# Optimization experiments

Hardware: AMD Instinct MI355X
Metric: run time of the kernel (lower is better)

The kernel has to match this reference:

```python
import jax, jax.numpy as jnp
import numpy as np

WIDTH = 256
FREQS = 10
INPUT_WIDTH = 3 + 3 * 2 * FREQS  # 63


def embed_point(point, freqs):
    # point: [N, 3] -> [N, 3*(1+2*freqs)]
    linear = point[..., None]                                  # [N, 3, 1]
    scales = jnp.exp2(jnp.arange(freqs, dtype=point.dtype))    # [freqs]
    angles = linear * scales                                   # [N, 3, freqs]
    emb = jnp.concatenate((linear, jnp.sin(angles), jnp.cos(angles)), axis=-1)
    return emb.reshape(*point.shape[:-1], 3 * (1 + 2 * freqs))


def _xavier(key, fan_in, fan_out):
    limit = jnp.sqrt(6.0 / (fan_in + fan_out)).astype(jnp.float32)
    return jax.random.uniform(key, (fan_in, fan_out), jnp.float32, -limit, limit)


def setup_inputs() -> dict:
    key = jax.random.key(0)
    keys = jax.random.split(key, 20)
    N = 524288
    point = jax.random.normal(keys[0], (N, 3), dtype=jnp.float32)
    dims = [
        (INPUT_WIDTH, WIDTH), (WIDTH, WIDTH), (WIDTH, WIDTH), (WIDTH, WIDTH),
        (WIDTH, WIDTH), (WIDTH + INPUT_WIDTH, WIDTH), (WIDTH, WIDTH),
        (WIDTH, WIDTH), (WIDTH, 4),
    ]
    inp = {"point": point}
    for i, (fi, fo) in enumerate(dims):
        inp[f"w{i}"] = _xavier(keys[1 + i], fi, fo)
        inp[f"b{i}"] = jnp.zeros((fo,), dtype=jnp.float32)
    return inp


def reference(point, w0, b0, w1, b1, w2, b2, w3, b3, w4, b4,
              w5, b5, w6, b6, w7, b7, w8, b8):
    inp = embed_point(point, FREQS)                 # [N, 63]
    x = jax.nn.relu(inp @ w0 + b0)
    x = jax.nn.relu(x @ w1 + b1)
    x = jax.nn.relu(x @ w2 + b2)
    x = jax.nn.relu(x @ w3 + b3)
    x = jax.nn.relu(x @ w4 + b4)
    x = jax.nn.relu(jnp.concatenate((x, inp), -1) @ w5 + b5)  # skip concat
    x = jax.nn.relu(x @ w6 + b6)
    x = jax.nn.relu(x @ w7 + b7)
    return x @ w8 + b8                              # [N, 4]
```

## Files before the change

kernel.cpp:

```cpp
#include <hip/hip_runtime.h>
#include <math.h>


typedef __attribute__((ext_vector_type(8))) short short8;
typedef __attribute__((ext_vector_type(4))) float f32x4;
typedef __attribute__((ext_vector_type(16))) float f32x16;

struct WPtrs { const float* w[8]; };
struct BPtrs { const float* b[8]; };

#define INV2PI 0.15915494309189533577f

#define PK_L0 0
#define PK_L1 16384
#define PK_L2 81920
#define PK_L3 147456
#define PK_L4 212992
#define PK_L5 278528
#define PK_L6 360448
#define PK_L7 425984
#define PK_W8 491520
#define PK_TOTAL 495616

__device__ __forceinline__ unsigned short f2bf(float v) {
  unsigned u = __float_as_uint(v);
  u = u + 0x7fffu + ((u >> 16) & 1u);
  return (unsigned short)(u >> 16);
}
__device__ __forceinline__ float bf_lo(unsigned u) { return __uint_as_float(u << 16); }
__device__ __forceinline__ float bf_hi(unsigned u) { return __uint_as_float(u & 0xffff0000u); }

__device__ __forceinline__ unsigned cvtpk(float a, float b) {
#if __has_builtin(__builtin_amdgcn_cvt_pk_bf16_f32)
  typedef __attribute__((ext_vector_type(2))) __bf16 bf16x2_t;
  bf16x2_t r = __builtin_amdgcn_cvt_pk_bf16_f32(a, b);
  return __builtin_bit_cast(unsigned, r);
#else
  unsigned ua = __float_as_uint(a);
  ua += 0x7fffu + ((ua >> 16) & 1u);
  unsigned ub = __float_as_uint(b);
  ub += 0x7fffu + ((ub >> 16) & 1u);
#if __has_builtin(__builtin_amdgcn_perm)
  return __builtin_amdgcn_perm(ub, ua, 0x07060302u);
#else
  return (ua >> 16) | (ub & 0xffff0000u);
#endif
#endif
}

__device__ __forceinline__ float fractf_(float x) {
#if __has_builtin(__builtin_amdgcn_fract_f32)
  return __builtin_amdgcn_fract_f32(x);
#else
  return x - floorf(x);
#endif
}
__device__ __forceinline__ float sin_rev(float rev) {
#if __has_builtin(__builtin_amdgcn_sinf)
  return __builtin_amdgcn_sinf(rev);
#else
  return __sinf(rev * 6.283185307179586f);
#endif
}

__device__ __forceinline__ float embval(int f, float c0, float c1, float c2,
                                        float x0, float x1, float x2) {
  if (f >= 63) return 0.0f;
  int d = (f >= 21 ? 1 : 0) + (f >= 42 ? 1 : 0);
  int r = f - d * 21;
  float c = (d == 0) ? c0 : (d == 1 ? c1 : c2);
  float x = (d == 0) ? x0 : (d == 1 ? x1 : x2);
  bool isc = r > 10;
  int e = isc ? (r - 11) : (r - 1);
  float rev = fractf_(ldexpf(x, e) + (isc ? 0.25f : 0.0f));
  float s = sin_rev(rev);
  return (r == 0) ? c : s;
}

__device__ __forceinline__ f32x16 mfma32(short8 a, short8 b, f32x16 c) {
  return __builtin_amdgcn_mfma_f32_32x32x16_bf16(a, b, c, 0, 0, 0);
}
__device__ __forceinline__ f32x4 mfma16(short8 a, short8 b, f32x4 c) {
  return __builtin_amdgcn_mfma_f32_16x16x32_bf16(a, b, c, 0, 0, 0);
}

__global__ void pack_weights(WPtrs W, const float* __restrict__ w8,
                             unsigned short* __restrict__ out) {
  int idx = blockIdx.x * 256 + threadIdx.x;
  if (idx >= PK_TOTAL) return;
  float v;
  if (idx >= PK_W8) {
    int t = idx - PK_W8;
    int j = t >> 8, k = t & 255;
    v = (j < 4) ? w8[k * 4 + j] : 0.0f;
  } else {
    int e = idx & 15;
    int blk = idx >> 4;
    int ch = blk & 255;
    int kkg = blk >> 8;
    int l, kk0;
    if      (kkg < 4)   { l = 0; kk0 = 0;   }
    else if (kkg < 20)  { l = 1; kk0 = 4;   }
    else if (kkg < 36)  { l = 2; kk0 = 20;  }
    else if (kkg < 52)  { l = 3; kk0 = 36;  }
    else if (kkg < 68)  { l = 4; kk0 = 52;  }
    else if (kkg < 88)  { l = 5; kk0 = 68;  }
    else if (kkg < 104) { l = 6; kk0 = 88;  }
    else                { l = 7; kk0 = 104; }
    int k = (kkg - kk0) * 16 + e;
    const int realK[8] = {63, 256, 256, 256, 256, 319, 256, 256};
    v = (k < realK[l]) ? W.w[l][k * 256 + ch] : 0.0f;
  }
  out[idx] = f2bf(v);
}

template <int KKA, int PAB, int KKB, bool RB>
__device__ __forceinline__ void do_layer32(
    const unsigned short* srcA, const unsigned short* srcB,
    const unsigned short* __restrict__ wblk,
    const float* __restrict__ bias,
    unsigned short* dst, int w, int n, int h, unsigned swz) {
  f32x16 acc[2][4];
#pragma unroll
  for (int mt = 0; mt < 2; ++mt)
#pragma unroll
    for (int q = 0; q < 4; ++q) {
      f32x4 bq = *reinterpret_cast<const f32x4*>(bias + w * 64 + mt * 32 + q * 8 + h * 4);
#pragma unroll
      for (int nt = 0; nt < 4; ++nt)
#pragma unroll
        for (int r = 0; r < 4; ++r)
          acc[mt][nt][q * 4 + r] = bq[r];
    }

  const char* wb = (const char*)wblk;
  const unsigned aoff = (unsigned)(((w * 64 + n) * 16 + h * 8) * 2);
  const char* rA = (const char*)srcA + (unsigned)(n * PAB);

#pragma unroll 4
  for (int kk = 0; kk < KKA; ++kk) {
    short8 a0 = *reinterpret_cast<const short8*>(wb + (aoff + (unsigned)(kk * 8192)));
    short8 a1 = *reinterpret_cast<const short8*>(wb + (aoff + (unsigned)(kk * 8192 + 1024)));
    unsigned off = ((unsigned)(kk * 32 + h * 16)) ^ swz;
    const char* p = rA + off;
    short8 b0 = *reinterpret_cast<const short8*>(p);
    short8 b1 = *reinterpret_cast<const short8*>(p + 32 * PAB);
    short8 b2 = *reinterpret_cast<const short8*>(p + 64 * PAB);
    short8 b3 = *reinterpret_cast<const short8*>(p + 96 * PAB);
    acc[0][0] = mfma32(a0, b0, acc[0][0]);
    acc[0][1] = mfma32(a0, b1, acc[0][1]);
    acc[0][2] = mfma32(a0, b2, acc[0][2]);
    acc[0][3] = mfma32(a0, b3, acc[0][3]);
    acc[1][0] = mfma32(a1, b0, acc[1][0]);
    acc[1][1] = mfma32(a1, b1, acc[1][1]);
    acc[1][2] = mfma32(a1, b2, acc[1][2]);
    acc[1][3] = mfma32(a1, b3, acc[1][3]);
  }
  if (KKB > 0) {
    const char* rB = (const char*)srcB + (unsigned)(n * 128);
#pragma unroll
    for (int kl = 0; kl < KKB; ++kl) {
      const char* ab2 = wb + (aoff + (unsigned)((KKA + kl) * 8192));
      short8 a0 = *reinterpret_cast<const short8*>(ab2);
      short8 a1 = *reinterpret_cast<const short8*>(ab2 + 1024);
      unsigned off = ((unsigned)(kl * 32 + h * 16)) ^ swz;
      const char* p = rB + off;
      short8 b0 = *reinterpret_cast<const short8*>(p);
      short8 b1 = *reinterpret_cast<const short8*>(p + 32 * 128);
      short8 b2 = *reinterpret_cast<const short8*>(p + 64 * 128);
      short8 b3 = *reinterpret_cast<const short8*>(p + 96 * 128);
      acc[0][0] = mfma32(a0, b0, acc[0][0]);
      acc[0][1] = mfma32(a0, b1, acc[0][1]);
      acc[0][2] = mfma32(a0, b2, acc[0][2]);
      acc[0][3] = mfma32(a0, b3, acc[0][3]);
      acc[1][0] = mfma32(a1, b0, acc[1][0]);
      acc[1][1] = mfma32(a1, b1, acc[1][1]);
      acc[1][2] = mfma32(a1, b2, acc[1][2]);
      acc[1][3] = mfma32(a1, b3, acc[1][3]);
    }
  }

  if (RB) __syncthreads();
  char* d0 = (char*)dst + (unsigned)(n * 512);
#pragma unroll
  for (int mt = 0; mt < 2; ++mt)
#pragma unroll
    for (int q = 0; q < 4; ++q) {
      unsigned soff = ((unsigned)(w * 128 + mt * 64 + q * 16 + h * 8)) ^ swz;
      char* sp = d0 + soff;
#pragma unroll
      for (int nt = 0; nt < 4; ++nt) {
        float x0 = fmaxf(acc[mt][nt][q * 4 + 0], 0.0f);
        float x1 = fmaxf(acc[mt][nt][q * 4 + 1], 0.0f);
        float x2 = fmaxf(acc[mt][nt][q * 4 + 2], 0.0f);
        float x3 = fmaxf(acc[mt][nt][q * 4 + 3], 0.0f);
        uint2 pr;
        pr.x = cvtpk(x0, x1);
        pr.y = cvtpk(x2, x3);
        *reinterpret_cast<uint2*>(sp + nt * 16384) = pr;
      }
    }
  __syncthreads();
}

__launch_bounds__(256, 2)
__global__ void mlp_mfma(const float* __restrict__ pts, long N,
                         BPtrs B, const float* __restrict__ b8,
                         const unsigned short* __restrict__ wpk,
                         float* __restrict__ out) {
  extern __shared__ unsigned short smem[];
  unsigned short* act = smem;
  unsigned short* emb = smem + 32768;
  const int tid = threadIdx.x;
  const int w = tid >> 6, lane = tid & 63;
  const int n = lane & 31, h = lane >> 5;
  const unsigned swz = (unsigned)((n & 7) << 4);
  const long pbase = (long)blockIdx.x * 128;

  {
    const int pt = tid >> 1, fg = tid & 1;
    const long pg = pbase + pt;
    float c0 = 0.f, c1 = 0.f, c2 = 0.f;
    if (pg < N) {
      const float* pp = pts + pg * 3;
      c0 = __builtin_nontemporal_load(pp);
      c1 = __builtin_nontemporal_load(pp + 1);
      c2 = __builtin_nontemporal_load(pp + 2);
    }
    float x0 = c0 * INV2PI, x1 = c1 * INV2PI, x2 = c2 * INV2PI;
    const unsigned sw = (unsigned)((pt & 7) << 4);
    char* rowp = (char*)emb + (unsigned)(pt * 128);
#pragma unroll
    for (int jb = 0; jb < 2; ++jb) {
      unsigned pk[8];
#pragma unroll
      for (int i = 0; i < 16; i += 2) {
        int f0 = fg * 32 + jb * 16 + i;
        float v0 = embval(f0,     c0, c1, c2, x0, x1, x2);
        float v1 = embval(f0 + 1, c0, c1, c2, x0, x1, x2);
        pk[i >> 1] = cvtpk(v0, v1);
      }
      unsigned base = (unsigned)(fg * 64 + jb * 32);
      *reinterpret_cast<uint4*>(rowp + (base ^ sw)) =
          uint4{pk[0], pk[1], pk[2], pk[3]};
      *reinterpret_cast<uint4*>(rowp + ((base + 16) ^ sw)) =
          uint4{pk[4], pk[5], pk[6], pk[7]};
    }
  }
  __syncthreads();

  do_layer32<4,  128, 0, false>(emb, nullptr, wpk + PK_L0, B.b[0], act, w, n, h, swz);
  do_layer32<16, 512, 0, true >(act, nullptr, wpk + PK_L1, B.b[1], act, w, n, h, swz);
  do_layer32<16, 512, 0, true >(act, nullptr, wpk + PK_L2, B.b[2], act, w, n, h, swz);
  do_layer32<16, 512, 0, true >(act, nullptr, wpk + PK_L3, B.b[3], act, w, n, h, swz);
  do_layer32<16, 512, 0, true >(act, nullptr, wpk + PK_L4, B.b[4], act, w, n, h, swz);
  do_layer32<16, 512, 4, true >(act, emb,     wpk + PK_L5, B.b[5], act, w, n, h, swz);
  do_layer32<16, 512, 0, true >(act, nullptr, wpk + PK_L6, B.b[6], act, w, n, h, swz);
  do_layer32<16, 512, 0, true >(act, nullptr, wpk + PK_L7, B.b[7], act, w, n, h, swz);

  {
    const int l16 = lane & 15, quad = lane >> 4;
    const unsigned short* w8b = wpk + PK_W8 + (unsigned)(l16 * 256 + quad * 8);
    short8 wf[8];
#pragma unroll
    for (int kk = 0; kk < 8; ++kk)
      wf[kk] = *reinterpret_cast<const short8*>(w8b + kk * 32);
    f32x4 bb = *reinterpret_cast<const f32x4*>(b8);
#pragma unroll
    for (int it = 0; it < 2; ++it) {
      const int pt = w * 32 + it * 16 + l16;
      const char* ba = (const char*)act + (unsigned)(pt * 512);
      f32x4 a4 = {0.f, 0.f, 0.f, 0.f};
#pragma unroll
      for (int kk = 0; kk < 8; ++kk) {
        unsigned off = ((unsigned)(kk * 64 + quad * 16)) ^ swz;
        short8 b = *reinterpret_cast<const short8*>(ba + off);
        a4 = mfma16(wf[kk], b, a4);
      }
      if (quad == 0) {
        long pg = pbase + pt;
        f32x4 v = a4 + bb;
        if (pg < N)
          __builtin_nontemporal_store(v, reinterpret_cast<f32x4*>(out + pg * 4));
      }
    }
  }
}

__device__ __forceinline__ unsigned pk2s(float a, float b) {
  return (unsigned)f2bf(a) | ((unsigned)f2bf(b) << 16);
}
__device__ __forceinline__ void fb_seg(const unsigned short* src, int kRows,
                                       const float* __restrict__ wr,
                                       int lane, int ps, float acc[4][16]) {
#pragma unroll 4
  for (int k = 0; k < kRows; ++k) {
    const float* p = wr + k * 256 + lane;
    float w0 = p[0], w1 = p[64], w2 = p[128], w3 = p[192];
    const uint4* xr = reinterpret_cast<const uint4*>(src + ((k << 6) + ps));
    uint4 q0 = xr[0], q1 = xr[1];
    float x[16];
    x[0] = bf_lo(q0.x);  x[1] = bf_hi(q0.x);  x[2] = bf_lo(q0.y);  x[3] = bf_hi(q0.y);
    x[4] = bf_lo(q0.z);  x[5] = bf_hi(q0.z);  x[6] = bf_lo(q0.w);  x[7] = bf_hi(q0.w);
    x[8] = bf_lo(q1.x);  x[9] = bf_hi(q1.x);  x[10] = bf_lo(q1.y); x[11] = bf_hi(q1.y);
    x[12] = bf_lo(q1.z); x[13] = bf_hi(q1.z); x[14] = bf_lo(q1.w); x[15] = bf_hi(q1.w);
#pragma unroll
    for (int pp = 0; pp < 16; ++pp) {
      acc[0][pp] = fmaf(w0, x[pp], acc[0][pp]);
      acc[1][pp] = fmaf(w1, x[pp], acc[1][pp]);
      acc[2][pp] = fmaf(w2, x[pp], acc[2][pp]);
      acc[3][pp] = fmaf(w3, x[pp], acc[3][pp]);
    }
  }
}
__device__ __forceinline__ void fb_layer(const unsigned short* srcA, int kA,
                                         const unsigned short* srcB, int kB,
                                         const float* wrA, const float* wrB,
                                         const float* bias,
                                         unsigned short* dst, int lane, int ps) {
  float acc[4][16];
#pragma unroll
  for (int jt = 0; jt < 4; ++jt) {
    float bb = bias[lane + (jt << 6)];
#pragma unroll
    for (int pp = 0; pp < 16; ++pp) acc[jt][pp] = bb;
  }
  fb_seg(srcA, kA, wrA, lane, ps, acc);
  if (srcB) fb_seg(srcB, kB, wrB, lane, ps, acc);
#pragma unroll
  for (int jt = 0; jt < 4; ++jt) {
    unsigned short* dr = dst + (((lane + (jt << 6)) << 6) + ps);
    float r[16];
#pragma unroll
    for (int pp = 0; pp < 16; ++pp) r[pp] = fmaxf(acc[jt][pp], 0.0f);
    uint4 a, b;
    a.x = pk2s(r[0], r[1]);   a.y = pk2s(r[2], r[3]);
    a.z = pk2s(r[4], r[5]);   a.w = pk2s(r[6], r[7]);
    b.x = pk2s(r[8], r[9]);   b.y = pk2s(r[10], r[11]);
    b.z = pk2s(r[12], r[13]); b.w = pk2s(r[14], r[15]);
    reinterpret_cast<uint4*>(dr)[0] = a;
    reinterpret_cast<uint4*>(dr)[1] = b;
  }
}
__launch_bounds__(256, 2)
__global__ void mlp_fallback(const float* __restrict__ pts, int N,
                             WPtrs W, BPtrs B,
                             const float* __restrict__ w8,
                             const float* __restrict__ b8,
                             float* __restrict__ out) {
  __shared__ unsigned short act[256 * 64];
  __shared__ unsigned short emb[64 * 64];
  const int lane = threadIdx.x & 63;
  const int ps = (threadIdx.x >> 6) << 4;
  const long pbase = (long)blockIdx.x * 64 + ps;
#pragma unroll
  for (int i = 0; i < 16; ++i) {
    int idx = (i << 6) + lane;
    int f = idx >> 4, pp = idx & 15;
    float v = 0.0f;
    if (f < 63) {
      float c = (pbase + pp < N) ? pts[(pbase + pp) * 3 + (f / 21)] : 0.0f;
      float x = c * INV2PI;
      v = embval(f, c, c, c, x, x, x);
    }
    emb[(f << 6) + ps + pp] = f2bf(v);
  }
  fb_layer(emb, 63, nullptr, 0, W.w[0], nullptr, B.b[0], act, lane, ps);
#pragma unroll 1
  for (int l = 1; l <= 4; ++l)
    fb_layer(act, 256, nullptr, 0, W.w[l], nullptr, B.b[l], act, lane, ps);
  fb_layer(act, 256, emb, 63, W.w[5], W.w[5] + 256 * 256, B.b[5], act, lane, ps);
#pragma unroll 1
  for (int l = 6; l <= 7; ++l)
    fb_layer(act, 256, nullptr, 0, W.w[l], nullptr, B.b[l], act, lane, ps);
  {
    const int pp = lane & 15, cc = lane >> 4;
    float a = b8[cc];
#pragma unroll 4
    for (int k = 0; k < 256; ++k)
      a = fmaf(bf_lo((unsigned)act[(k << 6) + ps + pp]), w8[(k << 2) + cc], a);
    if (pbase + pp < N) out[(pbase + pp) * 4 + cc] = a;
  }
}

extern "C" void kernel_launch(void* const* d_in, const int* in_sizes, int n_in,
                              void* d_out, int out_size, void* d_ws, size_t ws_size,
                              hipStream_t stream) {
  const float* pts = (const float*)d_in[0];
  WPtrs W; BPtrs B;
  for (int i = 0; i < 8; ++i) {
    W.w[i] = (const float*)d_in[1 + 2 * i];
    B.b[i] = (const float*)d_in[2 + 2 * i];
  }
  const float* w8 = (const float*)d_in[17];
  const float* b8 = (const float*)d_in[18];
  float* out = (float*)d_out;
  const long N = in_sizes[0] / 3;

  const size_t need = (size_t)PK_TOTAL * sizeof(unsigned short);
  if (ws_size >= need) {
    static hipError_t attr_err = hipFuncSetAttribute(
        reinterpret_cast<const void*>(mlp_mfma),
        hipFuncAttributeMaxDynamicSharedMemorySize, 81920);
    if (attr_err == hipSuccess) {
      unsigned short* wpk = (unsigned short*)d_ws;
      pack_weights<<<1936, 256, 0, stream>>>(W, w8, wpk);
      mlp_mfma<<<(int)((N + 127) / 128), 256, 81920, stream>>>(pts, N, B, b8, wpk, out);
      return;
    }
  }
  mlp_fallback<<<(int)((N + 63) / 64), 256, 0, stream>>>(pts, (int)N, W, B, w8, b8, out);
}
```

Measured before the change: 551.9 us.

## Split MLP tile across eight waves and ping-pong activation buffers

Doubles the block to 512 threads and splits each layer's output tile over a 4x2 wave grid, so each wave holds half as many accumulators. Activations now alternate between two LDS buffers, which drops the pre-writeback barrier in each layer. The embedding stage is also redistributed over four threads per point. In exchange, LDS per block grows to 144KB, which likely allows only one block per CU, and each weight fragment fetched from global memory feeds half as many MFMAs.

New measurement: 698.8 us. 26.6% more time.

```diff
diff --git a/kernel.cpp b/kernel.cpp
--- a/kernel.cpp
+++ b/kernel.cpp
@@ -114,28 +114,28 @@
   out[idx] = f2bf(v);
 }
 
-template <int KKA, int PAB, int KKB, bool RB>
+template <int KKA, int PAB, int KKB>
 __device__ __forceinline__ void do_layer32(
     const unsigned short* srcA, const unsigned short* srcB,
     const unsigned short* __restrict__ wblk,
     const float* __restrict__ bias,
-    unsigned short* dst, int w, int n, int h, unsigned swz) {
-  f32x16 acc[2][4];
+    unsigned short* dst, int wr, int wc, int n, int h, unsigned swz) {
+  f32x16 acc[2][2];
 #pragma unroll
   for (int mt = 0; mt < 2; ++mt)
 #pragma unroll
     for (int q = 0; q < 4; ++q) {
-      f32x4 bq = *reinterpret_cast<const f32x4*>(bias + w * 64 + mt * 32 + q * 8 + h * 4);
-#pragma unroll
-      for (int nt = 0; nt < 4; ++nt)
+      f32x4 bq = *reinterpret_cast<const f32x4*>(bias + wr * 64 + mt * 32 + q * 8 + h * 4);
+#pragma unroll
+      for (int nt = 0; nt < 2; ++nt)
 #pragma unroll
         for (int r = 0; r < 4; ++r)
           acc[mt][nt][q * 4 + r] = bq[r];
     }
 
   const char* wb = (const char*)wblk;
-  const unsigned aoff = (unsigned)(((w * 64 + n) * 16 + h * 8) * 2);
-  const char* rA = (const char*)srcA + (unsigned)(n * PAB);
+  const unsigned aoff = (unsigned)((wr * 64 + n) * 32 + h * 16);
+  const char* rA = (const char*)srcA + (unsigned)((wc * 64 + n) * PAB);
 
 #pragma unroll 4
   for (int kk = 0; kk < KKA; ++kk) {
@@ -145,19 +145,13 @@
     const char* p = rA + off;
     short8 b0 = *reinterpret_cast<const short8*>(p);
     short8 b1 = *reinterpret_cast<const short8*>(p + 32 * PAB);
-    short8 b2 = *reinterpret_cast<const short8*>(p + 64 * PAB);
-    short8 b3 = *reinterpret_cast<const short8*>(p + 96 * PAB);
     acc[0][0] = mfma32(a0, b0, acc[0][0]);
     acc[0][1] = mfma32(a0, b1, acc[0][1]);
-    acc[0][2] = mfma32(a0, b2, acc[0][2]);
-    acc[0][3] = mfma32(a0, b3, acc[0][3]);
     acc[1][0] = mfma32(a1, b0, acc[1][0]);
     acc[1][1] = mfma32(a1, b1, acc[1][1]);
-    acc[1][2] = mfma32(a1, b2, acc[1][2]);
-    acc[1][3] = mfma32(a1, b3, acc[1][3]);
   }
   if (KKB > 0) {
-    const char* rB = (const char*)srcB + (unsigned)(n * 128);
+    const char* rB = (const char*)srcB + (unsigned)((wc * 64 + n) * 128);
 #pragma unroll
     for (int kl = 0; kl < KKB; ++kl) {
       const char* ab2 = wb + (aoff + (unsigned)((KKA + kl) * 8192));
@@ -167,29 +161,22 @@
       const char* p = rB + off;
       short8 b0 = *reinterpret_cast<const short8*>(p);
       short8 b1 = *reinterpret_cast<const short8*>(p + 32 * 128);
-      short8 b2 = *reinterpret_cast<const short8*>(p + 64 * 128);
-      short8 b3 = *reinterpret_cast<const short8*>(p + 96 * 128);
       acc[0][0] = mfma32(a0, b0, acc[0][0]);
       acc[0][1] = mfma32(a0, b1, acc[0][1]);
-      acc[0][2] = mfma32(a0, b2, acc[0][2]);
-      acc[0][3] = mfma32(a0, b3, acc[0][3]);
       acc[1][0] = mfma32(a1, b0, acc[1][0]);
       acc[1][1] = mfma32(a1, b1, acc[1][1]);
-      acc[1][2] = mfma32(a1, b2, acc[1][2]);
-      acc[1][3] = mfma32(a1, b3, acc[1][3]);
-    }
-  }
-
-  if (RB) __syncthreads();
-  char* d0 = (char*)dst + (unsigned)(n * 512);
+    }
+  }
+
+  char* d0 = (char*)dst + (unsigned)((wc * 64 + n) * 512);
 #pragma unroll
   for (int mt = 0; mt < 2; ++mt)
 #pragma unroll
     for (int q = 0; q < 4; ++q) {
-      unsigned soff = ((unsigned)(w * 128 + mt * 64 + q * 16 + h * 8)) ^ swz;
+      unsigned soff = ((unsigned)(wr * 128 + mt * 64 + q * 16 + h * 8)) ^ swz;
       char* sp = d0 + soff;
 #pragma unroll
-      for (int nt = 0; nt < 4; ++nt) {
+      for (int nt = 0; nt < 2; ++nt) {
         float x0 = fmaxf(acc[mt][nt][q * 4 + 0], 0.0f);
         float x1 = fmaxf(acc[mt][nt][q * 4 + 1], 0.0f);
         float x2 = fmaxf(acc[mt][nt][q * 4 + 2], 0.0f);
@@ -203,22 +190,24 @@
   __syncthreads();
 }
 
-__launch_bounds__(256, 2)
+__launch_bounds__(512, 2)
 __global__ void mlp_mfma(const float* __restrict__ pts, long N,
                          BPtrs B, const float* __restrict__ b8,
                          const unsigned short* __restrict__ wpk,
                          float* __restrict__ out) {
   extern __shared__ unsigned short smem[];
-  unsigned short* act = smem;
-  unsigned short* emb = smem + 32768;
+  unsigned short* act0 = smem;
+  unsigned short* act1 = smem + 32768;
+  unsigned short* emb  = smem + 65536;
   const int tid = threadIdx.x;
   const int w = tid >> 6, lane = tid & 63;
   const int n = lane & 31, h = lane >> 5;
+  const int wr = w >> 1, wc = w & 1;
   const unsigned swz = (unsigned)((n & 7) << 4);
   const long pbase = (long)blockIdx.x * 128;
 
   {
-    const int pt = tid >> 1, fg = tid & 1;
+    const int pt = tid >> 2, fg = tid & 3;
     const long pg = pbase + pt;
     float c0 = 0.f, c1 = 0.f, c2 = 0.f;
     if (pg < N) {
@@ -228,35 +217,31 @@
       c2 = __builtin_nontemporal_load(pp + 2);
     }
     float x0 = c0 * INV2PI, x1 = c1 * INV2PI, x2 = c2 * INV2PI;
+    unsigned pk[8];
+#pragma unroll
+    for (int i = 0; i < 16; i += 2) {
+      int f0 = fg * 16 + i;
+      float v0 = embval(f0,     c0, c1, c2, x0, x1, x2);
+      float v1 = embval(f0 + 1, c0, c1, c2, x0, x1, x2);
+      pk[i >> 1] = cvtpk(v0, v1);
+    }
     const unsigned sw = (unsigned)((pt & 7) << 4);
     char* rowp = (char*)emb + (unsigned)(pt * 128);
-#pragma unroll
-    for (int jb = 0; jb < 2; ++jb) {
-      unsigned pk[8];
-#pragma unroll
-      for (int i = 0; i < 16; i += 2) {
-        int f0 = fg * 32 + jb * 16 + i;
-        float v0 = embval(f0,     c0, c1, c2, x0, x1, x2);
-        float v1 = embval(f0 + 1, c0, c1, c2, x0, x1, x2);
-        pk[i >> 1] = cvtpk(v0, v1);
-      }
-      unsigned base = (unsigned)(fg * 64 + jb * 32);
-      *reinterpret_cast<uint4*>(rowp + (base ^ sw)) =
-          uint4{pk[0], pk[1], pk[2], pk[3]};
-      *reinterpret_cast<uint4*>(rowp + ((base + 16) ^ sw)) =
-          uint4{pk[4], pk[5], pk[6], pk[7]};
-    }
+    *reinterpret_cast<uint4*>(rowp + (((unsigned)(fg * 32)) ^ sw)) =
+        uint4{pk[0], pk[1], pk[2], pk[3]};
+    *reinterpret_cast<uint4*>(rowp + (((unsigned)(fg * 32 + 16)) ^ sw)) =
+        uint4{pk[4], pk[5], pk[6], pk[7]};
   }
   __syncthreads();
 
-  do_layer32<4,  128, 0, false>(emb, nullptr, wpk + PK_L0, B.b[0], act, w, n, h, swz);
-  do_layer32<16, 512, 0, true >(act, nullptr, wpk + PK_L1, B.b[1], act, w, n, h, swz);
-  do_layer32<16, 512, 0, true >(act, nullptr, wpk + PK_L2, B.b[2], act, w, n, h, swz);
-  do_layer32<16, 512, 0, true >(act, nullptr, wpk + PK_L3, B.b[3], act, w, n, h, swz);
-  do_layer32<16, 512, 0, true >(act, nullptr, wpk + PK_L4, B.b[4], act, w, n, h, swz);
-  do_layer32<16, 512, 4, true >(act, emb,     wpk + PK_L5, B.b[5], act, w, n, h, swz);
-  do_layer32<16, 512, 0, true >(act, nullptr, wpk + PK_L6, B.b[6], act, w, n, h, swz);
-  do_layer32<16, 512, 0, true >(act, nullptr, wpk + PK_L7, B.b[7], act, w, n, h, swz);
+  do_layer32<4,  128, 0>(emb,  nullptr, wpk + PK_L0, B.b[0], act0, wr, wc, n, h, swz);
+  do_layer32<16, 512, 0>(act0, nullptr, wpk + PK_L1, B.b[1], act1, wr, wc, n, h, swz);
+  do_layer32<16, 512, 0>(act1, nullptr, wpk + PK_L2, B.b[2], act0, wr, wc, n, h, swz);
+  do_layer32<16, 512, 0>(act0, nullptr, wpk + PK_L3, B.b[3], act1, wr, wc, n, h, swz);
+  do_layer32<16, 512, 0>(act1, nullptr, wpk + PK_L4, B.b[4], act0, wr, wc, n, h, swz);
+  do_layer32<16, 512, 4>(act0, emb,     wpk + PK_L5, B.b[5], act1, wr, wc, n, h, swz);
+  do_layer32<16, 512, 0>(act1, nullptr, wpk + PK_L6, B.b[6], act0, wr, wc, n, h, swz);
+  do_layer32<16, 512, 0>(act0, nullptr, wpk + PK_L7, B.b[7], act1, wr, wc, n, h, swz);
 
   {
     const int l16 = lane & 15, quad = lane >> 4;
@@ -266,23 +251,20 @@
     for (int kk = 0; kk < 8; ++kk)
       wf[kk] = *reinterpret_cast<const short8*>(w8b + kk * 32);
     f32x4 bb = *reinterpret_cast<const f32x4*>(b8);
-#pragma unroll
-    for (int it = 0; it < 2; ++it) {
-      const int pt = w * 32 + it * 16 + l16;
-      const char* ba = (const char*)act + (unsigned)(pt * 512);
-      f32x4 a4 = {0.f, 0.f, 0.f, 0.f};
-#pragma unroll
-      for (int kk = 0; kk < 8; ++kk) {
-        unsigned off = ((unsigned)(kk * 64 + quad * 16)) ^ swz;
-        short8 b = *reinterpret_cast<const short8*>(ba + off);
-        a4 = mfma16(wf[kk], b, a4);
-      }
-      if (quad == 0) {
-        long pg = pbase + pt;
-        f32x4 v = a4 + bb;
-        if (pg < N)
-          __builtin_nontemporal_store(v, reinterpret_cast<f32x4*>(out + pg * 4));
-      }
+    const int pt = w * 16 + l16;
+    const char* ba = (const char*)act1 + (unsigned)(pt * 512);
+    f32x4 a4 = {0.f, 0.f, 0.f, 0.f};
+#pragma unroll
+    for (int kk = 0; kk < 8; ++kk) {
+      unsigned off = ((unsigned)(kk * 64 + quad * 16)) ^ swz;
+      short8 b = *reinterpret_cast<const short8*>(ba + off);
+      a4 = mfma16(wf[kk], b, a4);
+    }
+    if (quad == 0) {
+      long pg = pbase + pt;
+      f32x4 v = a4 + bb;
+      if (pg < N)
+        __builtin_nontemporal_store(v, reinterpret_cast<f32x4*>(out + pg * 4));
     }
   }
 }
@@ -401,11 +383,11 @@
   if (ws_size >= need) {
     static hipError_t attr_err = hipFuncSetAttribute(
         reinterpret_cast<const void*>(mlp_mfma),
-        hipFuncAttributeMaxDynamicSharedMemorySize, 81920);
+        hipFuncAttributeMaxDynamicSharedMemorySize, 147456);
     if (attr_err == hipSuccess) {
       unsigned short* wpk = (unsigned short*)d_ws;
       pack_weights<<<1936, 256, 0, stream>>>(W, w8, wpk);
-      mlp_mfma<<<(int)((N + 127) / 128), 256, 81920, stream>>>(pts, N, B, b8, wpk, out);
+      mlp_mfma<<<(int)((N + 127) / 128), 512, 147456, stream>>>(pts, N, B, b8, wpk, out);
       return;
     }
   }
```

## Split warps into 2x2 grid over output channels and points in MLP layers

Applied to the files above, without the earlier changes.

Changes the per-wave tile in each layer from 64 channels x 128 points to 128 channels x 64 points, arranging the four waves as a 2x2 grid. Each k-step now loads four weight fragments from global/L2 and two activation fragments from LDS instead of two and four. That halves LDS activation reads per MFMA but doubles per-wave weight fragment loads from global memory, which may add latency and cache pressure.

After: 635.7 us. 15.2% more time.

```diff
diff --git a/kernel.cpp b/kernel.cpp
--- a/kernel.cpp
+++ b/kernel.cpp
@@ -119,77 +119,78 @@
     const unsigned short* srcA, const unsigned short* srcB,
     const unsigned short* __restrict__ wblk,
     const float* __restrict__ bias,
-    unsigned short* dst, int w, int n, int h, unsigned swz) {
-  f32x16 acc[2][4];
-#pragma unroll
-  for (int mt = 0; mt < 2; ++mt)
+    unsigned short* dst, int wr, int wc, int n, int h, unsigned swz) {
+  f32x16 acc[4][2];
+#pragma unroll
+  for (int mt = 0; mt < 4; ++mt)
 #pragma unroll
     for (int q = 0; q < 4; ++q) {
-      f32x4 bq = *reinterpret_cast<const f32x4*>(bias + w * 64 + mt * 32 + q * 8 + h * 4);
-#pragma unroll
-      for (int nt = 0; nt < 4; ++nt)
+      f32x4 bq = *reinterpret_cast<const f32x4*>(bias + wr * 128 + mt * 32 + q * 8 + h * 4);
+#pragma unroll
+      for (int nt = 0; nt < 2; ++nt)
 #pragma unroll
         for (int r = 0; r < 4; ++r)
           acc[mt][nt][q * 4 + r] = bq[r];
     }
 
   const char* wb = (const char*)wblk;
-  const unsigned aoff = (unsigned)(((w * 64 + n) * 16 + h * 8) * 2);
-  const char* rA = (const char*)srcA + (unsigned)(n * PAB);
-
-#pragma unroll 4
+  const unsigned aoff = (unsigned)((wr * 128 + n) * 32 + h * 16);
+  const char* rA = (const char*)srcA + (unsigned)((wc * 64 + n) * PAB);
+
+#pragma unroll 2
   for (int kk = 0; kk < KKA; ++kk) {
-    short8 a0 = *reinterpret_cast<const short8*>(wb + (aoff + (unsigned)(kk * 8192)));
-    short8 a1 = *reinterpret_cast<const short8*>(wb + (aoff + (unsigned)(kk * 8192 + 1024)));
+    const char* ap = wb + (aoff + (unsigned)(kk * 8192));
+    short8 a0 = *reinterpret_cast<const short8*>(ap);
+    short8 a1 = *reinterpret_cast<const short8*>(ap + 1024);
+    short8 a2 = *reinterpret_cast<const short8*>(ap + 2048);
+    short8 a3 = *reinterpret_cast<const short8*>(ap + 3072);
     unsigned off = ((unsigned)(kk * 32 + h * 16)) ^ swz;
     const char* p = rA + off;
     short8 b0 = *reinterpret_cast<const short8*>(p);
     short8 b1 = *reinterpret_cast<const short8*>(p + 32 * PAB);
-    short8 b2 = *reinterpret_cast<const short8*>(p + 64 * PAB);
-    short8 b3 = *reinterpret_cast<const short8*>(p + 96 * PAB);
     acc[0][0] = mfma32(a0, b0, acc[0][0]);
     acc[0][1] = mfma32(a0, b1, acc[0][1]);
-    acc[0][2] = mfma32(a0, b2, acc[0][2]);
-    acc[0][3] = mfma32(a0, b3, acc[0][3]);
     acc[1][0] = mfma32(a1, b0, acc[1][0]);
     acc[1][1] = mfma32(a1, b1, acc[1][1]);
-    acc[1][2] = mfma32(a1, b2, acc[1][2]);
-    acc[1][3] = mfma32(a1, b3, acc[1][3]);
+    acc[2][0] = mfma32(a2, b0, acc[2][0]);
+    acc[2][1] = mfma32(a2, b1, acc[2][1]);
+    acc[3][0] = mfma32(a3, b0, acc[3][0]);
+    acc[3][1] = mfma32(a3, b1, acc[3][1]);
   }
   if (KKB > 0) {
-    const char* rB = (const char*)srcB + (unsigned)(n * 128);
+    const char* rB = (const char*)srcB + (unsigned)((wc * 64 + n) * 128);
 #pragma unroll
     for (int kl = 0; kl < KKB; ++kl) {
-      const char* ab2 = wb + (aoff + (unsigned)((KKA + kl) * 8192));
-      short8 a0 = *reinterpret_cast<const short8*>(ab2);
-      short8 a1 = *reinterpret_cast<const short8*>(ab2 + 1024);
+      const char* ap = wb + (aoff + (unsigned)((KKA + kl) * 8192));
+      short8 a0 = *reinterpret_cast<const short8*>(ap);
+      short8 a1 = *reinterpret_cast<const short8*>(ap + 1024);
+      short8 a2 = *reinterpret_cast<const short8*>(ap + 2048);
+      short8 a3 = *reinterpret_cast<const short8*>(ap + 3072);
       unsigned off = ((unsigned)(kl * 32 + h * 16)) ^ swz;
       const char* p = rB + off;
       short8 b0 = *reinterpret_cast<const short8*>(p);
       short8 b1 = *reinterpret_cast<const short8*>(p + 32 * 128);
-      short8 b2 = *reinterpret_cast<const short8*>(p + 64 * 128);
-      short8 b3 = *reinterpret_cast<const short8*>(p + 96 * 128);
       acc[0][0] = mfma32(a0, b0, acc[0][0]);
       acc[0][1] = mfma32(a0, b1, acc[0][1]);
-      acc[0][2] = mfma32(a0, b2, acc[0][2]);
-      acc[0][3] = mfma32(a0, b3, acc[0][3]);
       acc[1][0] = mfma32(a1, b0, acc[1][0]);
       acc[1][1] = mfma32(a1, b1, acc[1][1]);
-      acc[1][2] = mfma32(a1, b2, acc[1][2]);
-      acc[1][3] = mfma32(a1, b3, acc[1][3]);
+      acc[2][0] = mfma32(a2, b0, acc[2][0]);
+      acc[2][1] = mfma32(a2, b1, acc[2][1]);
+      acc[3][0] = mfma32(a3, b0, acc[3][0]);
+      acc[3][1] = mfma32(a3, b1, acc[3][1]);
     }
   }
 
   if (RB) __syncthreads();
-  char* d0 = (char*)dst + (unsigned)(n * 512);
-#pragma unroll
-  for (int mt = 0; mt < 2; ++mt)
+  char* d0 = (char*)dst + (unsigned)((wc * 64 + n) * 512);
+#pragma unroll
+  for (int mt = 0; mt < 4; ++mt)
 #pragma unroll
     for (int q = 0; q < 4; ++q) {
-      unsigned soff = ((unsigned)(w * 128 + mt * 64 + q * 16 + h * 8)) ^ swz;
+      unsigned soff = ((unsigned)(wr * 256 + mt * 64 + q * 16 + h * 8)) ^ swz;
       char* sp = d0 + soff;
 #pragma unroll
-      for (int nt = 0; nt < 4; ++nt) {
+      for (int nt = 0; nt < 2; ++nt) {
         float x0 = fmaxf(acc[mt][nt][q * 4 + 0], 0.0f);
         float x1 = fmaxf(acc[mt][nt][q * 4 + 1], 0.0f);
         float x2 = fmaxf(acc[mt][nt][q * 4 + 2], 0.0f);
@@ -214,6 +215,7 @@
   const int tid = threadIdx.x;
   const int w = tid >> 6, lane = tid & 63;
   const int n = lane & 31, h = lane >> 5;
+  const int wr = w >> 1, wc = w & 1;
   const unsigned swz = (unsigned)((n & 7) << 4);
   const long pbase = (long)blockIdx.x * 128;
 
@@ -249,14 +251,14 @@
   }
   __syncthreads();
 
-  do_layer32<4,  128, 0, false>(emb, nullptr, wpk + PK_L0, B.b[0], act, w, n, h, swz);
-  do_layer32<16, 512, 0, true >(act, nullptr, wpk + PK_L1, B.b[1], act, w, n, h, swz);
-  do_layer32<16, 512, 0, true >(act, nullptr, wpk + PK_L2, B.b[2], act, w, n, h, swz);
-  do_layer32<16, 512, 0, true >(act, nullptr, wpk + PK_L3, B.b[3], act, w, n, h, swz);
-  do_layer32<16, 512, 0, true >(act, nullptr, wpk + PK_L4, B.b[4], act, w, n, h, swz);
-  do_layer32<16, 512, 4, true >(act, emb,     wpk + PK_L5, B.b[5], act, w, n, h, swz);
-  do_layer32<16, 512, 0, true >(act, nullptr, wpk + PK_L6, B.b[6], act, w, n, h, swz);
-  do_layer32<16, 512, 0, true >(act, nullptr, wpk + PK_L7, B.b[7], act, w, n, h, swz);
+  do_layer32<4,  128, 0, false>(emb, nullptr, wpk + PK_L0, B.b[0], act, wr, wc, n, h, swz);
+  do_layer32<16, 512, 0, true >(act, nullptr, wpk + PK_L1, B.b[1], act, wr, wc, n, h, swz);
+  do_layer32<16, 512, 0, true >(act, nullptr, wpk + PK_L2, B.b[2], act, wr, wc, n, h, swz);
+  do_layer32<16, 512, 0, true >(act, nullptr, wpk + PK_L3, B.b[3], act, wr, wc, n, h, swz);
+  do_layer32<16, 512, 0, true >(act, nullptr, wpk + PK_L4, B.b[4], act, wr, wc, n, h, swz);
+  do_layer32<16, 512, 4, true >(act, emb,     wpk + PK_L5, B.b[5], act, wr, wc, n, h, swz);
+  do_layer32<16, 512, 0, true >(act, nullptr, wpk + PK_L6, B.b[6], act, wr, wc, n, h, swz);
+  do_layer32<16, 512, 0, true >(act, nullptr, wpk + PK_L7, B.b[7], act, wr, wc, n, h, swz);
 
   {
     const int l16 = lane & 15, quad = lane >> 4;
```
